# Kernel optimization log

Measured on AMD Instinct MI355X. Metric: run time of the kernel, lower is better.

Reference implementation:

```python
import jax, jax.numpy as jnp
import numpy as np

B, N, T = 64, 300, 30
BIG = jnp.float32(1e18)


def box_xywh_to_xyxy(b):
    x, y, w, h = b[..., 0], b[..., 1], b[..., 2], b[..., 3]
    return jnp.stack([x, y, x + w, y + h], axis=-1)


def giou_matrix(a, b):
    # a: [..., N, 4] xyxy, b: [..., M, 4] xyxy -> [..., N, M]
    area_a = (a[..., 2] - a[..., 0]) * (a[..., 3] - a[..., 1])
    area_b = (b[..., 2] - b[..., 0]) * (b[..., 3] - b[..., 1])
    lt = jnp.maximum(a[..., :, None, :2], b[..., None, :, :2])
    rb = jnp.minimum(a[..., :, None, 2:], b[..., None, :, 2:])
    wh = jnp.clip(rb - lt, 0.0)
    inter = wh[..., 0] * wh[..., 1]
    union = area_a[..., :, None] + area_b[..., None, :] - inter
    iou = inter / union
    ltc = jnp.minimum(a[..., :, None, :2], b[..., None, :, :2])
    rbc = jnp.maximum(a[..., :, None, 2:], b[..., None, :, 2:])
    whc = jnp.clip(rbc - ltc, 0.0)
    areac = whc[..., 0] * whc[..., 1]
    return iou - (areac - union) / areac


def giou_pair(a, b):
    # elementwise giou of paired boxes: a,b [..., 4] xyxy -> [...]
    area_a = (a[..., 2] - a[..., 0]) * (a[..., 3] - a[..., 1])
    area_b = (b[..., 2] - b[..., 0]) * (b[..., 3] - b[..., 1])
    lt = jnp.maximum(a[..., :2], b[..., :2])
    rb = jnp.minimum(a[..., 2:], b[..., 2:])
    wh = jnp.clip(rb - lt, 0.0)
    inter = wh[..., 0] * wh[..., 1]
    union = area_a + area_b - inter
    iou = inter / union
    ltc = jnp.minimum(a[..., :2], b[..., :2])
    rbc = jnp.maximum(a[..., 2:], b[..., 2:])
    whc = jnp.clip(rbc - ltc, 0.0)
    areac = whc[..., 0] * whc[..., 1]
    return iou - (areac - union) / areac


def lsa_col4row(cost):
    # Hungarian (shortest augmenting path, as in scipy.linear_sum_assignment)
    # cost: [R, C] with R <= C (minimization). Returns col4row [R] int32:
    # the column matched to each row.
    R, C = cost.shape

    def solve_row(carry, row):
        u, v, col4row, row4col = carry

        def search_cond(s):
            return s[6] < 0

        def search_body(s):
            cur_i, minVal, SR, SC, spc, path, sink = s
            SR = SR.at[cur_i].set(True)
            red = minVal + cost[cur_i] - u[cur_i] - v  # reduced costs [C]
            remaining = ~SC
            better = remaining & (red < spc)
            spc = jnp.where(better, red, spc)
            path = jnp.where(better, cur_i, path)
            masked = jnp.where(remaining, spc, BIG)
            j = jnp.argmin(masked)
            minVal = masked[j]
            SC = SC.at[j].set(True)
            r = row4col[j]
            hit = r < 0
            sink = jnp.where(hit, j, jnp.int32(-1))
            cur_i = jnp.where(hit, cur_i, r)
            return cur_i, minVal, SR, SC, spc, path, sink

        init = (row, jnp.float32(0.0),
                jnp.zeros((R,), bool), jnp.zeros((C,), bool),
                jnp.full((C,), BIG), jnp.zeros((C,), jnp.int32), jnp.int32(-1))
        cur_i, minVal, SR, SC, spc, path, sink = jax.lax.while_loop(
            search_cond, search_body, init)

        # dual updates
        u = u + jnp.where(SR & (jnp.arange(R) != row),
                          minVal - spc[jnp.clip(col4row, 0, C - 1)], 0.0)
        u = u.at[row].add(minVal)
        v = v - jnp.where(SC, minVal - spc, 0.0)

        # augment along alternating path back from sink
        def aug_cond(s):
            return ~s[3]

        def aug_body(s):
            j, c4r, r4c, _ = s
            i = path[j]
            r4c = r4c.at[j].set(i)
            nj = c4r[i]
            c4r = c4r.at[i].set(j)
            return nj, c4r, r4c, i == row

        _, col4row, row4col, _ = jax.lax.while_loop(
            aug_cond, aug_body, (sink, col4row, row4col, jnp.array(False)))
        return (u, v, col4row, row4col), jnp.int32(0)

    init = (jnp.zeros((R,), jnp.float32), jnp.zeros((C,), jnp.float32),
            jnp.full((R,), -1, jnp.int32), jnp.full((C,), -1, jnp.int32))
    (u, v, col4row, row4col), _ = jax.lax.scan(solve_row, init, jnp.arange(R, dtype=jnp.int32))
    return col4row


def setup_inputs() -> dict:
    key = jax.random.key(0)
    k1, k2, k3 = jax.random.split(key, 3)
    pred_boxes = jax.random.uniform(k1, (B, N, 4), dtype=jnp.float32)
    # probabilities in (0, 1): output of a sigmoid head, fed directly to BCE
    pred_classes = jax.random.uniform(k2, (B, N), dtype=jnp.float32,
                                      minval=1e-4, maxval=1.0 - 1e-4)
    targets = jax.random.uniform(k3, (B, T, 4), dtype=jnp.float32)
    return {"pred_boxes": pred_boxes, "pred_classes": pred_classes,
            "targets": targets}


def reference(pred_boxes, pred_classes, targets):
    # --- matcher (no_grad in the original) ---
    pb = jax.lax.stop_gradient(pred_boxes)
    pc = jax.lax.stop_gradient(pred_classes)
    tg = jax.lax.stop_gradient(targets)
    giou_part = -giou_matrix(box_xywh_to_xyxy(pb), box_xywh_to_xyxy(tg))  # [B,N,T]
    class_part = -pc[..., None]                                            # [B,N,1]
    bbox_part = jnp.sum(jnp.abs(pb[:, :, None, :] - tg[:, None, :, :]), -1)  # L1 cdist
    cost = class_part + giou_part + bbox_part                               # [B,N,T]
    # scipy transposes when rows > cols; boxes_idx = sorted matched row indices
    col4row = jax.vmap(lsa_col4row)(jnp.swapaxes(cost, 1, 2))  # [B,T] pred idx per target
    boxes_idx = jnp.sort(col4row, axis=-1)

    num_boxes = jnp.float32(B * T)
    barange = jnp.arange(B)[:, None]

    # --- classification: BCE with 1.0 at matched queries ---
    labels = jnp.zeros_like(pred_classes).at[barange, boxes_idx].set(1.0)
    p = pred_classes
    bce = -(labels * jnp.clip(jnp.log(p), -100.0)
            + (1.0 - labels) * jnp.clip(jnp.log(1.0 - p), -100.0))
    loss_classification = bce.mean()

    # --- boxes: L1 + GIoU on matched (sorted-idx) pairs ---
    src = pred_boxes[barange, boxes_idx]  # [B,T,4]
    loss_bbox = jnp.abs(src - targets).sum() / num_boxes
    g = giou_pair(box_xywh_to_xyxy(src), box_xywh_to_xyxy(targets))  # [B,T]
    loss_giou = (1.0 - g).sum() / num_boxes

    return jnp.stack([loss_classification, loss_bbox, loss_giou])
```

## Files before the change

kernel.cpp:

```cpp
#include <hip/hip_runtime.h>

#define BB 64
#define NN 300
#define TT 30
#define BIGF 1e18f
#define KPL 5

__device__ __forceinline__ float giou_xyxy(float ax0, float ay0, float ax1, float ay1, float area_a,
                                           float bx0, float by0, float bx1, float by1, float area_b) {
    float ltx = fmaxf(ax0, bx0), lty = fmaxf(ay0, by0);
    float rbx = fminf(ax1, bx1), rby = fminf(ay1, by1);
    float w = fmaxf(__fsub_rn(rbx, ltx), 0.0f);
    float h = fmaxf(__fsub_rn(rby, lty), 0.0f);
    float inter = __fmul_rn(w, h);
    float uni = __fsub_rn(__fadd_rn(area_a, area_b), inter);
    float iou = inter / uni;
    float cx0 = fminf(ax0, bx0), cy0 = fminf(ay0, by0);
    float cx1 = fmaxf(ax1, bx1), cy1 = fmaxf(ay1, by1);
    float cw = fmaxf(__fsub_rn(cx1, cx0), 0.0f);
    float ch = fmaxf(__fsub_rn(cy1, cy0), 0.0f);
    float areac = __fmul_rn(cw, ch);
    return __fsub_rn(iou, __fsub_rn(areac, uni) / areac);
}

__device__ __forceinline__ int   rl_i(int v, int l)   { return __builtin_amdgcn_readlane(v, l); }
__device__ __forceinline__ float rl_f(float v, int l) { return __int_as_float(__builtin_amdgcn_readlane(__float_as_int(v), l)); }

__device__ __forceinline__ float dpp_min_f32(float g) {
#define SM(ctrl)                                                                                          \
    {                                                                                                     \
        float o = __int_as_float(__builtin_amdgcn_update_dpp(__float_as_int(g), __float_as_int(g),        \
                                                             ctrl, 0xF, 0xF, false));                     \
        g = fminf(g, o);                                                                                  \
    }
    SM(0x111) SM(0x112) SM(0x114) SM(0x118) SM(0x142) SM(0x143)
#undef SM
    return rl_f(g, 63);
}

__device__ __forceinline__ int first_match_j(const float m[KPL], float gmin) {
    unsigned long long b0 = __ballot(m[0] == gmin);
    unsigned long long b1 = __ballot(m[1] == gmin);
    unsigned long long b2 = __ballot(m[2] == gmin);
    unsigned long long b3 = __ballot(m[3] == gmin);
    unsigned long long b4 = __ballot(m[4] == gmin);
    if (b0) return       __builtin_ctzll(b0);
    if (b1) return  64 + __builtin_ctzll(b1);
    if (b2) return 128 + __builtin_ctzll(b2);
    if (b3) return 192 + __builtin_ctzll(b3);
    return        256 + __builtin_ctzll(b4);
}

__device__ __forceinline__ int sel5(const int a[KPL], int k) {
    int r = a[0];
    r = (k == 1) ? a[1] : r;
    r = (k == 2) ? a[2] : r;
    r = (k == 3) ? a[3] : r;
    r = (k == 4) ? a[4] : r;
    return r;
}

__launch_bounds__(256, 1)
__global__ void detcrit_kernel(const float* __restrict__ pred_boxes,
                               const float* __restrict__ pred_classes,
                               const float* __restrict__ targets,
                               float* __restrict__ out) {
    const int b = blockIdx.x;
    const int tid = threadIdx.x;
    const int lane = tid & 63;
    const int wave = tid >> 6;

    __shared__ float s_pb[NN][5];
    __shared__ float s_px[NN][5];
    __shared__ float s_pa[NN];
    __shared__ float s_pc[NN];
    __shared__ float s_tb[TT][4];
    __shared__ float s_tx[TT][4];
    __shared__ float s_ta[TT];
    __shared__ float s_cost[TT][NN];
    __shared__ float s_rmv[TT];
    __shared__ int   s_rmj[TT];
    __shared__ int   s_sorted[TT];
    __shared__ unsigned char s_lab[NN];
    __shared__ float s_rc[4], s_rb[4], s_rg[4];

    const float4* pbg = (const float4*)(pred_boxes + (size_t)b * NN * 4);
    const float4* tgg = (const float4*)(targets + (size_t)b * TT * 4);
    const float*  pcg = pred_classes + (size_t)b * NN;

    float rbx[KPL], rby[KPL], rbw[KPL], rbh[KPL];
    float rx2[KPL], ry2[KPL], rpa[KPL], rpc[KPL];
    #pragma unroll
    for (int k = 0; k < KPL; ++k) {
        int jc = lane + 64 * k;
        if (jc < NN) {
            float4 v = pbg[jc];
            rbx[k] = v.x; rby[k] = v.y; rbw[k] = v.z; rbh[k] = v.w;
            rx2[k] = __fadd_rn(v.x, v.z);
            ry2[k] = __fadd_rn(v.y, v.w);
            rpa[k] = __fmul_rn(__fsub_rn(rx2[k], v.x), __fsub_rn(ry2[k], v.y));
            rpc[k] = pcg[jc];
        } else {
            rbx[k] = rby[k] = rbw[k] = rbh[k] = 0.0f;
            rx2[k] = ry2[k] = rpa[k] = rpc[k] = 0.0f;
        }
    }

    for (int n = tid; n < NN; n += 256) {
        float4 v = pbg[n];
        s_pb[n][0] = v.x; s_pb[n][1] = v.y; s_pb[n][2] = v.z; s_pb[n][3] = v.w;
        float x2 = __fadd_rn(v.x, v.z), y2 = __fadd_rn(v.y, v.w);
        s_px[n][0] = v.x; s_px[n][1] = v.y; s_px[n][2] = x2; s_px[n][3] = y2;
        s_pa[n] = __fmul_rn(__fsub_rn(x2, v.x), __fsub_rn(y2, v.y));
        s_pc[n] = pcg[n];
        s_lab[n] = 0;
    }
    if (tid < TT) {
        float4 v = tgg[tid];
        s_tb[tid][0] = v.x; s_tb[tid][1] = v.y; s_tb[tid][2] = v.z; s_tb[tid][3] = v.w;
        float x2 = __fadd_rn(v.x, v.z), y2 = __fadd_rn(v.y, v.w);
        s_tx[tid][0] = v.x; s_tx[tid][1] = v.y; s_tx[tid][2] = x2; s_tx[tid][3] = y2;
        s_ta[tid] = __fmul_rn(__fsub_rn(x2, v.x), __fsub_rn(y2, v.y));
    }
    __syncthreads();

    for (int t = wave; t < TT; t += 4) {
        float tbx = s_tb[t][0], tby = s_tb[t][1], tbw = s_tb[t][2], tbh = s_tb[t][3];
        float tx2 = __fadd_rn(tbx, tbw), ty2 = __fadd_rn(tby, tbh);
        float tta = __fmul_rn(__fsub_rn(tx2, tbx), __fsub_rn(ty2, tby));

        float m[KPL];
        #pragma unroll
        for (int k = 0; k < KPL; ++k) {
            int jc = lane + 64 * k;
            float cv = BIGF;
            if (jc < NN) {
                float g = giou_xyxy(rbx[k], rby[k], rx2[k], ry2[k], rpa[k],
                                    tbx, tby, tx2, ty2, tta);
                float l1 = __fadd_rn(__fadd_rn(__fadd_rn(
                               fabsf(__fsub_rn(rbx[k], tbx)),
                               fabsf(__fsub_rn(rby[k], tby))),
                               fabsf(__fsub_rn(rbw[k], tbw))),
                               fabsf(__fsub_rn(rbh[k], tbh)));
                cv = __fadd_rn(__fadd_rn(-rpc[k], -g), l1);
                s_cost[t][jc] = cv;
            }
            m[k] = cv;
        }
        float gm = fminf(fminf(fminf(m[0], m[1]), fminf(m[2], m[3])), m[4]);
        gm = dpp_min_f32(gm);
        int bj = first_match_j(m, gm);
        if (lane == 0) { s_rmv[t] = gm; s_rmj[t] = bj; }
    }
    __syncthreads();

    if (tid < 64) {
        float u_reg = 0.0f;
        int   c4r_reg = -1;

        float vdual[KPL];
        float spc[KPL];
        int   path[KPL];
        int   r4c[KPL];
        #pragma unroll
        for (int k = 0; k < KPL; ++k) { vdual[k] = 0.0f; r4c[k] = -1; }
        const int SCinit = (lane < (NN - 64 * (KPL - 1))) ? 0 : (1 << (KPL - 1));

        unsigned assignedm = 0;
        {
            float rmv_reg = (lane < TT) ? s_rmv[lane] : 0.0f;
            int   rmj_reg = (lane < TT) ? s_rmj[lane] : 0;
            u_reg = (lane < TT) ? rmv_reg : 0.0f;
            for (int t = 0; t < TT; ++t) {
                int j = rl_i(rmj_reg, t);
                int owner = j & 63, k2 = j >> 6;
                int rcur = rl_i(sel5(r4c, k2), owner);
                if (rcur < 0) {
                    if (lane == owner) {
                        if      (k2 == 0) r4c[0] = t;
                        else if (k2 == 1) r4c[1] = t;
                        else if (k2 == 2) r4c[2] = t;
                        else if (k2 == 3) r4c[3] = t;
                        else              r4c[4] = t;
                    }
                    if (lane == t) c4r_reg = j;
                    assignedm |= (1u << t);
                }
            }
        }

        for (int row = 0; row < TT; ++row) {
            if ((assignedm >> row) & 1u) continue;

            #pragma unroll
            for (int k = 0; k < KPL; ++k) { spc[k] = BIGF; path[k] = 0; }
            int      SC = SCinit;
            unsigned srm = 0;
            float    minVal = 0.0f;
            int      cur_i = row;
            int      sink = -1;

            for (int guard = 0; guard < NN + 2; ++guard) {
                srm |= (1u << cur_i);
                const float* crow = &s_cost[cur_i][0];
                float cld[KPL];
                #pragma unroll
                for (int k = 0; k < KPL; ++k)
                    cld[k] = (!((SC >> k) & 1)) ? crow[lane + 64 * k] : 0.0f;
                float u_cur = rl_f(u_reg, cur_i);

                float m[KPL];
                #pragma unroll
                for (int k = 0; k < KPL; ++k) {
                    if (!((SC >> k) & 1)) {
                        float red = __fsub_rn(__fsub_rn(__fadd_rn(minVal, cld[k]), u_cur), vdual[k]);
                        if (red < spc[k]) { spc[k] = red; path[k] = cur_i; }
                        m[k] = spc[k];
                    } else {
                        m[k] = BIGF;
                    }
                }
                float gm = fminf(fminf(fminf(m[0], m[1]), fminf(m[2], m[3])), m[4]);
                gm = dpp_min_f32(gm);
                minVal = gm;
                int bj = first_match_j(m, gm);

                int owner = bj & 63;
                int k2    = bj >> 6;
                if (lane == owner) SC |= (1 << k2);
                int r = rl_i(sel5(r4c, k2), owner);
                if (r < 0) { sink = bj; break; }
                cur_i = r;
            }

            {
                int cj = c4r_reg;
                cj = (cj < 0) ? 0 : ((cj > NN - 1) ? NN - 1 : cj);
                int ou = cj & 63, ku = cj >> 6;
                float g0 = __shfl(spc[0], ou);
                float g1 = __shfl(spc[1], ou);
                float g2 = __shfl(spc[2], ou);
                float g3 = __shfl(spc[3], ou);
                float g4 = __shfl(spc[4], ou);
                float selspc = (ku == 0) ? g0 : (ku == 1) ? g1 : (ku == 2) ? g2 : (ku == 3) ? g3 : g4;
                if (lane < TT) {
                    if (lane == row) {
                        u_reg = __fadd_rn(u_reg, minVal);
                    } else if ((srm >> lane) & 1u) {
                        u_reg = __fadd_rn(u_reg, __fsub_rn(minVal, selspc));
                    }
                }
            }
            #pragma unroll
            for (int k = 0; k < KPL; ++k) {
                if (((SC >> k) & 1) && (lane + 64 * k) < NN)
                    vdual[k] = __fsub_rn(vdual[k], __fsub_rn(minVal, spc[k]));
            }

            int j = sink;
            for (int it = 0; it < TT + 2 && sink >= 0; ++it) {
                int oa = j & 63, ka = j >> 6;
                int i = rl_i(sel5(path, ka), oa);
                if (lane == oa) {
                    if      (ka == 0) r4c[0] = i;
                    else if (ka == 1) r4c[1] = i;
                    else if (ka == 2) r4c[2] = i;
                    else if (ka == 3) r4c[3] = i;
                    else              r4c[4] = i;
                }
                int nj = rl_i(c4r_reg, i);
                if (lane == i) c4r_reg = j;
                if (i == row) break;
                j = nj;
            }
        }

        {
            int myv = c4r_reg;
            int rank = 0;
            #pragma unroll
            for (int mq = 0; mq < TT; ++mq) {
                int vm = rl_i(c4r_reg, mq);
                rank += (vm < myv) ? 1 : 0;
            }
            if (lane < TT) {
                s_sorted[rank] = myv;
                s_lab[myv] = 1;
            }
        }
    }
    __syncthreads();

    float acc_c = 0.0f, acc_b = 0.0f, acc_g = 0.0f;
    for (int n = tid; n < NN; n += 256) {
        float p = s_pc[n];
        float lp = fmaxf(logf(p), -100.0f);
        float lq = fmaxf(logf(__fsub_rn(1.0f, p)), -100.0f);
        acc_c += s_lab[n] ? -lp : -lq;
    }
    if (tid < TT) {
        int t = tid;
        int idx = s_sorted[t];
        acc_b = fabsf(s_pb[idx][0] - s_tb[t][0]) + fabsf(s_pb[idx][1] - s_tb[t][1])
              + fabsf(s_pb[idx][2] - s_tb[t][2]) + fabsf(s_pb[idx][3] - s_tb[t][3]);
        float g = giou_xyxy(s_px[idx][0], s_px[idx][1], s_px[idx][2], s_px[idx][3], s_pa[idx],
                            s_tx[t][0], s_tx[t][1], s_tx[t][2], s_tx[t][3], s_ta[t]);
        acc_g = 1.0f - g;
    }
    for (int off = 32; off; off >>= 1) {
        acc_c += __shfl_down(acc_c, off);
        acc_b += __shfl_down(acc_b, off);
        acc_g += __shfl_down(acc_g, off);
    }
    if ((tid & 63) == 0) { s_rc[wave] = acc_c; s_rb[wave] = acc_b; s_rg[wave] = acc_g; }
    __syncthreads();
    if (tid == 0) {
        float c  = s_rc[0] + s_rc[1] + s_rc[2] + s_rc[3];
        float bx = s_rb[0] + s_rb[1] + s_rb[2] + s_rb[3];
        float g  = s_rg[0] + s_rg[1] + s_rg[2] + s_rg[3];
        atomicAdd(&out[0], c  * (1.0f / (float)(BB * NN)));
        atomicAdd(&out[1], bx * (1.0f / (float)(BB * TT)));
        atomicAdd(&out[2], g  * (1.0f / (float)(BB * TT)));
    }
}

extern "C" void kernel_launch(void* const* d_in, const int* in_sizes, int n_in,
                              void* d_out, int out_size, void* d_ws, size_t ws_size,
                              hipStream_t stream) {
    const float* pred_boxes   = (const float*)d_in[0];
    const float* pred_classes = (const float*)d_in[1];
    const float* targets      = (const float*)d_in[2];
    float* out = (float*)d_out;

    hipMemsetAsync(out, 0, 3 * sizeof(float), stream);
    detcrit_kernel<<<BB, 256, 0, stream>>>(pred_boxes, pred_classes, targets, out);
}
```

Measured before the change: 88.67 us.

## Drop shared-memory staging and atomics; finish with a second reduction kernel

The per-prediction shared arrays are removed; the loss epilogue now runs in wave 0 only, reusing register-held box and class data and gathering matched boxes with lane shuffles. Waves 1-3 exit after the cost matrix is built, and the final block-level syncthreads and LDS reduction go away. The memset and global atomics are replaced by per-block partials in workspace plus a tiny finish kernel. This adds a second kernel launch, which may cost more than the removed memset and atomics.

New measurement: 88.33 us. Within noise of the previous version (-0.4%).

```diff
diff --git a/kernel.cpp b/kernel.cpp
--- a/kernel.cpp
+++ b/kernel.cpp
@@ -60,20 +60,30 @@
     return r;
 }
 
+__device__ __forceinline__ float gather_attr(const float a[KPL], int srcLane, int k) {
+    float t0 = __shfl(a[0], srcLane);
+    float t1 = __shfl(a[1], srcLane);
+    float t2 = __shfl(a[2], srcLane);
+    float t3 = __shfl(a[3], srcLane);
+    float t4 = __shfl(a[4], srcLane);
+    float r = t0;
+    r = (k == 1) ? t1 : r;
+    r = (k == 2) ? t2 : r;
+    r = (k == 3) ? t3 : r;
+    r = (k == 4) ? t4 : r;
+    return r;
+}
+
 __launch_bounds__(256, 1)
 __global__ void detcrit_kernel(const float* __restrict__ pred_boxes,
                                const float* __restrict__ pred_classes,
                                const float* __restrict__ targets,
-                               float* __restrict__ out) {
+                               float* __restrict__ ws) {
     const int b = blockIdx.x;
     const int tid = threadIdx.x;
     const int lane = tid & 63;
     const int wave = tid >> 6;
 
-    __shared__ float s_pb[NN][5];
-    __shared__ float s_px[NN][5];
-    __shared__ float s_pa[NN];
-    __shared__ float s_pc[NN];
     __shared__ float s_tb[TT][4];
     __shared__ float s_tx[TT][4];
     __shared__ float s_ta[TT];
@@ -81,8 +91,6 @@
     __shared__ float s_rmv[TT];
     __shared__ int   s_rmj[TT];
     __shared__ int   s_sorted[TT];
-    __shared__ unsigned char s_lab[NN];
-    __shared__ float s_rc[4], s_rb[4], s_rg[4];
 
     const float4* pbg = (const float4*)(pred_boxes + (size_t)b * NN * 4);
     const float4* tgg = (const float4*)(targets + (size_t)b * TT * 4);
@@ -105,16 +113,6 @@
             rx2[k] = ry2[k] = rpa[k] = rpc[k] = 0.0f;
         }
     }
-
-    for (int n = tid; n < NN; n += 256) {
-        float4 v = pbg[n];
-        s_pb[n][0] = v.x; s_pb[n][1] = v.y; s_pb[n][2] = v.z; s_pb[n][3] = v.w;
-        float x2 = __fadd_rn(v.x, v.z), y2 = __fadd_rn(v.y, v.w);
-        s_px[n][0] = v.x; s_px[n][1] = v.y; s_px[n][2] = x2; s_px[n][3] = y2;
-        s_pa[n] = __fmul_rn(__fsub_rn(x2, v.x), __fsub_rn(y2, v.y));
-        s_pc[n] = pcg[n];
-        s_lab[n] = 0;
-    }
     if (tid < TT) {
         float4 v = tgg[tid];
         s_tb[tid][0] = v.x; s_tb[tid][1] = v.y; s_tb[tid][2] = v.z; s_tb[tid][3] = v.w;
@@ -153,157 +151,174 @@
         if (lane == 0) { s_rmv[t] = gm; s_rmj[t] = bj; }
     }
     __syncthreads();
-
-    if (tid < 64) {
-        float u_reg = 0.0f;
-        int   c4r_reg = -1;
-
-        float vdual[KPL];
-        float spc[KPL];
-        int   path[KPL];
-        int   r4c[KPL];
+    if (wave != 0) return;
+
+    float u_reg = 0.0f;
+    int   c4r_reg = -1;
+
+    float vdual[KPL];
+    float spc[KPL];
+    int   path[KPL];
+    int   r4c[KPL];
+    #pragma unroll
+    for (int k = 0; k < KPL; ++k) { vdual[k] = 0.0f; r4c[k] = -1; }
+    const int SCinit = (lane < (NN - 64 * (KPL - 1))) ? 0 : (1 << (KPL - 1));
+
+    unsigned assignedm = 0;
+    {
+        float rmv_reg = (lane < TT) ? s_rmv[lane] : 0.0f;
+        int   rmj_reg = (lane < TT) ? s_rmj[lane] : 0;
+        u_reg = (lane < TT) ? rmv_reg : 0.0f;
+        for (int t = 0; t < TT; ++t) {
+            int j = rl_i(rmj_reg, t);
+            int owner = j & 63, k2 = j >> 6;
+            int rcur = rl_i(sel5(r4c, k2), owner);
+            if (rcur < 0) {
+                if (lane == owner) {
+                    if      (k2 == 0) r4c[0] = t;
+                    else if (k2 == 1) r4c[1] = t;
+                    else if (k2 == 2) r4c[2] = t;
+                    else if (k2 == 3) r4c[3] = t;
+                    else              r4c[4] = t;
+                }
+                if (lane == t) c4r_reg = j;
+                assignedm |= (1u << t);
+            }
+        }
+    }
+
+    for (int row = 0; row < TT; ++row) {
+        if ((assignedm >> row) & 1u) continue;
+
         #pragma unroll
-        for (int k = 0; k < KPL; ++k) { vdual[k] = 0.0f; r4c[k] = -1; }
-        const int SCinit = (lane < (NN - 64 * (KPL - 1))) ? 0 : (1 << (KPL - 1));
-
-        unsigned assignedm = 0;
-        {
-            float rmv_reg = (lane < TT) ? s_rmv[lane] : 0.0f;
-            int   rmj_reg = (lane < TT) ? s_rmj[lane] : 0;
-            u_reg = (lane < TT) ? rmv_reg : 0.0f;
-            for (int t = 0; t < TT; ++t) {
-                int j = rl_i(rmj_reg, t);
-                int owner = j & 63, k2 = j >> 6;
-                int rcur = rl_i(sel5(r4c, k2), owner);
-                if (rcur < 0) {
-                    if (lane == owner) {
-                        if      (k2 == 0) r4c[0] = t;
-                        else if (k2 == 1) r4c[1] = t;
-                        else if (k2 == 2) r4c[2] = t;
-                        else if (k2 == 3) r4c[3] = t;
-                        else              r4c[4] = t;
-                    }
-                    if (lane == t) c4r_reg = j;
-                    assignedm |= (1u << t);
-                }
-            }
-        }
-
-        for (int row = 0; row < TT; ++row) {
-            if ((assignedm >> row) & 1u) continue;
-
+        for (int k = 0; k < KPL; ++k) { spc[k] = BIGF; path[k] = 0; }
+        int      SC = SCinit;
+        unsigned srm = 0;
+        float    minVal = 0.0f;
+        int      cur_i = row;
+        int      sink = -1;
+
+        for (int guard = 0; guard < NN + 2; ++guard) {
+            srm |= (1u << cur_i);
+            const float* crow = &s_cost[cur_i][0];
+            float cld[KPL];
             #pragma unroll
-            for (int k = 0; k < KPL; ++k) { spc[k] = BIGF; path[k] = 0; }
-            int      SC = SCinit;
-            unsigned srm = 0;
-            float    minVal = 0.0f;
-            int      cur_i = row;
-            int      sink = -1;
-
-            for (int guard = 0; guard < NN + 2; ++guard) {
-                srm |= (1u << cur_i);
-                const float* crow = &s_cost[cur_i][0];
-                float cld[KPL];
-                #pragma unroll
-                for (int k = 0; k < KPL; ++k)
-                    cld[k] = (!((SC >> k) & 1)) ? crow[lane + 64 * k] : 0.0f;
-                float u_cur = rl_f(u_reg, cur_i);
-
-                float m[KPL];
-                #pragma unroll
-                for (int k = 0; k < KPL; ++k) {
-                    if (!((SC >> k) & 1)) {
-                        float red = __fsub_rn(__fsub_rn(__fadd_rn(minVal, cld[k]), u_cur), vdual[k]);
-                        if (red < spc[k]) { spc[k] = red; path[k] = cur_i; }
-                        m[k] = spc[k];
-                    } else {
-                        m[k] = BIGF;
-                    }
-                }
-                float gm = fminf(fminf(fminf(m[0], m[1]), fminf(m[2], m[3])), m[4]);
-                gm = dpp_min_f32(gm);
-                minVal = gm;
-                int bj = first_match_j(m, gm);
-
-                int owner = bj & 63;
-                int k2    = bj >> 6;
-                if (lane == owner) SC |= (1 << k2);
-                int r = rl_i(sel5(r4c, k2), owner);
-                if (r < 0) { sink = bj; break; }
-                cur_i = r;
-            }
-
-            {
-                int cj = c4r_reg;
-                cj = (cj < 0) ? 0 : ((cj > NN - 1) ? NN - 1 : cj);
-                int ou = cj & 63, ku = cj >> 6;
-                float g0 = __shfl(spc[0], ou);
-                float g1 = __shfl(spc[1], ou);
-                float g2 = __shfl(spc[2], ou);
-                float g3 = __shfl(spc[3], ou);
-                float g4 = __shfl(spc[4], ou);
-                float selspc = (ku == 0) ? g0 : (ku == 1) ? g1 : (ku == 2) ? g2 : (ku == 3) ? g3 : g4;
-                if (lane < TT) {
-                    if (lane == row) {
-                        u_reg = __fadd_rn(u_reg, minVal);
-                    } else if ((srm >> lane) & 1u) {
-                        u_reg = __fadd_rn(u_reg, __fsub_rn(minVal, selspc));
-                    }
-                }
-            }
+            for (int k = 0; k < KPL; ++k)
+                cld[k] = (!((SC >> k) & 1)) ? crow[lane + 64 * k] : 0.0f;
+            float u_cur = rl_f(u_reg, cur_i);
+
+            float m[KPL];
             #pragma unroll
             for (int k = 0; k < KPL; ++k) {
-                if (((SC >> k) & 1) && (lane + 64 * k) < NN)
-                    vdual[k] = __fsub_rn(vdual[k], __fsub_rn(minVal, spc[k]));
-            }
-
-            int j = sink;
-            for (int it = 0; it < TT + 2 && sink >= 0; ++it) {
-                int oa = j & 63, ka = j >> 6;
-                int i = rl_i(sel5(path, ka), oa);
-                if (lane == oa) {
-                    if      (ka == 0) r4c[0] = i;
-                    else if (ka == 1) r4c[1] = i;
-                    else if (ka == 2) r4c[2] = i;
-                    else if (ka == 3) r4c[3] = i;
-                    else              r4c[4] = i;
+                if (!((SC >> k) & 1)) {
+                    float red = __fsub_rn(__fsub_rn(__fadd_rn(minVal, cld[k]), u_cur), vdual[k]);
+                    if (red < spc[k]) { spc[k] = red; path[k] = cur_i; }
+                    m[k] = spc[k];
+                } else {
+                    m[k] = BIGF;
                 }
-                int nj = rl_i(c4r_reg, i);
-                if (lane == i) c4r_reg = j;
-                if (i == row) break;
-                j = nj;
-            }
+            }
+            float gm = fminf(fminf(fminf(m[0], m[1]), fminf(m[2], m[3])), m[4]);
+            gm = dpp_min_f32(gm);
+            minVal = gm;
+            int bj = first_match_j(m, gm);
+
+            int owner = bj & 63;
+            int k2    = bj >> 6;
+            if (lane == owner) SC |= (1 << k2);
+            int r = rl_i(sel5(r4c, k2), owner);
+            if (r < 0) { sink = bj; break; }
+            cur_i = r;
         }
 
         {
-            int myv = c4r_reg;
-            int rank = 0;
-            #pragma unroll
-            for (int mq = 0; mq < TT; ++mq) {
-                int vm = rl_i(c4r_reg, mq);
-                rank += (vm < myv) ? 1 : 0;
-            }
+            int cj = c4r_reg;
+            cj = (cj < 0) ? 0 : ((cj > NN - 1) ? NN - 1 : cj);
+            int ou = cj & 63, ku = cj >> 6;
+            float g0 = __shfl(spc[0], ou);
+            float g1 = __shfl(spc[1], ou);
+            float g2 = __shfl(spc[2], ou);
+            float g3 = __shfl(spc[3], ou);
+            float g4 = __shfl(spc[4], ou);
+            float selspc = (ku == 0) ? g0 : (ku == 1) ? g1 : (ku == 2) ? g2 : (ku == 3) ? g3 : g4;
             if (lane < TT) {
-                s_sorted[rank] = myv;
-                s_lab[myv] = 1;
-            }
-        }
-    }
-    __syncthreads();
-
-    float acc_c = 0.0f, acc_b = 0.0f, acc_g = 0.0f;
-    for (int n = tid; n < NN; n += 256) {
-        float p = s_pc[n];
-        float lp = fmaxf(logf(p), -100.0f);
-        float lq = fmaxf(logf(__fsub_rn(1.0f, p)), -100.0f);
-        acc_c += s_lab[n] ? -lp : -lq;
-    }
-    if (tid < TT) {
-        int t = tid;
-        int idx = s_sorted[t];
-        acc_b = fabsf(s_pb[idx][0] - s_tb[t][0]) + fabsf(s_pb[idx][1] - s_tb[t][1])
-              + fabsf(s_pb[idx][2] - s_tb[t][2]) + fabsf(s_pb[idx][3] - s_tb[t][3]);
-        float g = giou_xyxy(s_px[idx][0], s_px[idx][1], s_px[idx][2], s_px[idx][3], s_pa[idx],
+                if (lane == row) {
+                    u_reg = __fadd_rn(u_reg, minVal);
+                } else if ((srm >> lane) & 1u) {
+                    u_reg = __fadd_rn(u_reg, __fsub_rn(minVal, selspc));
+                }
+            }
+        }
+        #pragma unroll
+        for (int k = 0; k < KPL; ++k) {
+            if (((SC >> k) & 1) && (lane + 64 * k) < NN)
+                vdual[k] = __fsub_rn(vdual[k], __fsub_rn(minVal, spc[k]));
+        }
+
+        int j = sink;
+        for (int it = 0; it < TT + 2 && sink >= 0; ++it) {
+            int oa = j & 63, ka = j >> 6;
+            int i = rl_i(sel5(path, ka), oa);
+            if (lane == oa) {
+                if      (ka == 0) r4c[0] = i;
+                else if (ka == 1) r4c[1] = i;
+                else if (ka == 2) r4c[2] = i;
+                else if (ka == 3) r4c[3] = i;
+                else              r4c[4] = i;
+            }
+            int nj = rl_i(c4r_reg, i);
+            if (lane == i) c4r_reg = j;
+            if (i == row) break;
+            j = nj;
+        }
+    }
+
+    unsigned labm = 0;
+    for (int t = 0; t < TT; ++t) {
+        int j = rl_i(c4r_reg, t);
+        if ((j & 63) == lane) labm |= 1u << (j >> 6);
+    }
+    float acc_c = 0.0f;
+    #pragma unroll
+    for (int k = 0; k < KPL; ++k) {
+        int jc = lane + 64 * k;
+        if (jc < NN) {
+            float p = rpc[k];
+            float lp = fmaxf(logf(p), -100.0f);
+            float lq = fmaxf(logf(__fsub_rn(1.0f, p)), -100.0f);
+            acc_c += ((labm >> k) & 1u) ? -lp : -lq;
+        }
+    }
+
+    {
+        int myv = c4r_reg;
+        int rank = 0;
+        #pragma unroll
+        for (int mq = 0; mq < TT; ++mq) {
+            int vm = rl_i(c4r_reg, mq);
+            rank += (vm < myv) ? 1 : 0;
+        }
+        volatile int* vs = s_sorted;
+        if (lane < TT) vs[rank] = myv;
+    }
+    volatile int* vs = s_sorted;
+    int srt = vs[(lane < TT) ? lane : 0];
+
+    int ow = srt & 63, kk = srt >> 6;
+    float gx  = gather_attr(rbx, ow, kk);
+    float gy  = gather_attr(rby, ow, kk);
+    float gw  = gather_attr(rbw, ow, kk);
+    float gh  = gather_attr(rbh, ow, kk);
+    float gx2 = gather_attr(rx2, ow, kk);
+    float gy2 = gather_attr(ry2, ow, kk);
+    float ga  = gather_attr(rpa, ow, kk);
+
+    float acc_b = 0.0f, acc_g = 0.0f;
+    if (lane < TT) {
+        int t = lane;
+        acc_b = fabsf(gx - s_tb[t][0]) + fabsf(gy - s_tb[t][1])
+              + fabsf(gw - s_tb[t][2]) + fabsf(gh - s_tb[t][3]);
+        float g = giou_xyxy(gx, gy, gx2, gy2, ga,
                             s_tx[t][0], s_tx[t][1], s_tx[t][2], s_tx[t][3], s_ta[t]);
         acc_g = 1.0f - g;
     }
@@ -312,15 +327,28 @@
         acc_b += __shfl_down(acc_b, off);
         acc_g += __shfl_down(acc_g, off);
     }
-    if ((tid & 63) == 0) { s_rc[wave] = acc_c; s_rb[wave] = acc_b; s_rg[wave] = acc_g; }
-    __syncthreads();
-    if (tid == 0) {
-        float c  = s_rc[0] + s_rc[1] + s_rc[2] + s_rc[3];
-        float bx = s_rb[0] + s_rb[1] + s_rb[2] + s_rb[3];
-        float g  = s_rg[0] + s_rg[1] + s_rg[2] + s_rg[3];
-        atomicAdd(&out[0], c  * (1.0f / (float)(BB * NN)));
-        atomicAdd(&out[1], bx * (1.0f / (float)(BB * TT)));
-        atomicAdd(&out[2], g  * (1.0f / (float)(BB * TT)));
+    if (lane == 0) {
+        float* wsf = ws + b * 4;
+        wsf[0] = acc_c;
+        wsf[1] = acc_b;
+        wsf[2] = acc_g;
+    }
+}
+
+__global__ void finish_kernel(const float* __restrict__ ws, float* __restrict__ out) {
+    int lane = threadIdx.x;
+    float c = ws[lane * 4 + 0];
+    float bx = ws[lane * 4 + 1];
+    float g = ws[lane * 4 + 2];
+    for (int off = 32; off; off >>= 1) {
+        c  += __shfl_down(c, off);
+        bx += __shfl_down(bx, off);
+        g  += __shfl_down(g, off);
+    }
+    if (lane == 0) {
+        out[0] = c  * (1.0f / (float)(BB * NN));
+        out[1] = bx * (1.0f / (float)(BB * TT));
+        out[2] = g  * (1.0f / (float)(BB * TT));
     }
 }
 
@@ -331,7 +359,8 @@
     const float* pred_classes = (const float*)d_in[1];
     const float* targets      = (const float*)d_in[2];
     float* out = (float*)d_out;
-
-    hipMemsetAsync(out, 0, 3 * sizeof(float), stream);
-    detcrit_kernel<<<BB, 256, 0, stream>>>(pred_boxes, pred_classes, targets, out);
-}
+    float* ws  = (float*)d_ws;
+
+    detcrit_kernel<<<BB, 256, 0, stream>>>(pred_boxes, pred_classes, targets, ws);
+    finish_kernel<<<1, 64, 0, stream>>>(ws, out);
+}
```
